# Performance work log

Measured on AMD Instinct MI355X. Metric: run time of the kernel, lower is better.

Reference implementation:

```python
import jax, jax.numpy as jnp
import numpy as np

MARGIN = 0.3
BIG = 9999999.0


def setup_inputs() -> dict:
    key = jax.random.key(0)
    k1, k2 = jax.random.split(key)
    emb = jax.random.normal(k1, (4096, 2048), dtype=jnp.float32)
    label = jax.random.randint(k2, (4096,), 0, 64, dtype=jnp.int64 if jax.config.jax_enable_x64 else jnp.int32)
    return {"emb": emb, "label": label}


def euclidean_dist(x, y):
    xx = jnp.sum(x * x, axis=1, keepdims=True)          # [m,1]
    yy = jnp.sum(y * y, axis=1, keepdims=True).T        # [1,n]
    dist = xx + yy - 2.0 * (x @ y.T)                    # [m,n]
    return jnp.sqrt(jnp.clip(dist, 1e-12, None))


def reference(emb, label):
    mat_dist = euclidean_dist(emb, emb)                 # [N,N]
    mat_sim = (label[:, None] == label[None, :]).astype(mat_dist.dtype)
    # batch-hard mining: top-1 of masked sorts == masked max / min reductions
    dist_ap = jnp.max(mat_dist - BIG * (1.0 - mat_sim), axis=1)  # hardest positive
    dist_an = jnp.min(mat_dist + BIG * mat_sim, axis=1)          # hardest negative
    # MarginRankingLoss(dist_an, dist_ap, y=1): mean(relu(margin - (dist_an - dist_ap)))
    loss = jnp.mean(jax.nn.relu(MARGIN - (dist_an - dist_ap)))
    prec = jnp.mean((dist_an > dist_ap).astype(jnp.float32))
    return (loss, prec)
```

## Files before the change

kernel.cpp:

```cpp
#include <hip/hip_runtime.h>

#define N_ROWS 4096
#define D_K    2048
#define BM 256
#define BK 64
#define NT (D_K / BK)
#define MARGIN 0.3f

typedef unsigned short u16;
typedef __attribute__((ext_vector_type(8))) short bf16x8;
typedef __attribute__((ext_vector_type(4))) float f32x4;

__device__ __forceinline__ void stage16(const u16* src, u16* dst) {
    __builtin_amdgcn_global_load_lds((const __attribute__((address_space(1))) unsigned int*)src,
                                     (__attribute__((address_space(3))) unsigned int*)dst, 16, 0, 0);
}

__device__ __forceinline__ u16 f2bf(float f) {
    unsigned u = __float_as_uint(f);
    u += 0x7fffu + ((u >> 16) & 1u);
    return (u16)(u >> 16);
}

__global__ __launch_bounds__(256) void prep_kernel(
    const float* __restrict__ emb, u16* __restrict__ embB,
    float* __restrict__ xx, unsigned* __restrict__ ap2, unsigned* __restrict__ an2)
{
    const int row = blockIdx.x;
    const int t = threadIdx.x;
    const float4* src = (const float4*)(emb + (size_t)row * D_K);
    ushort4* dst = (ushort4*)(embB + (size_t)row * D_K);
    float s = 0.f;
#pragma unroll
    for (int i = 0; i < 2; ++i) {
        float4 v = src[t + i * 256];
        s = fmaf(v.x, v.x, s);
        s = fmaf(v.y, v.y, s);
        s = fmaf(v.z, v.z, s);
        s = fmaf(v.w, v.w, s);
        ushort4 o;
        o.x = f2bf(v.x); o.y = f2bf(v.y); o.z = f2bf(v.z); o.w = f2bf(v.w);
        dst[t + i * 256] = o;
    }
#pragma unroll
    for (int off = 32; off >= 1; off >>= 1) s += __shfl_down(s, off, 64);
    __shared__ float red[4];
    if ((t & 63) == 0) red[t >> 6] = s;
    __syncthreads();
    if (t == 0) {
        xx[row] = red[0] + red[1] + red[2] + red[3];
        ap2[row] = 0u;
        an2[row] = 0x7f7fffffu;
    }
}

#define MM(mi, ni, ai, bi) \
    acc[mi][ni] = __builtin_amdgcn_mfma_f32_16x16x32_bf16(aq[ai][0], bq[bi][0], acc[mi][ni], 0, 0, 0); \
    acc[mi][ni] = __builtin_amdgcn_mfma_f32_16x16x32_bf16(aq[ai][1], bq[bi][1], acc[mi][ni], 0, 0, 0);

#define LDv(p) (*(const bf16x8*)(p))

#define STAGE_A(b, h, c, kt) stage16(gA + ((h) * 2 + (c)) * g64 + (kt), lA + ((b) * 16384 + ((h) * 128 + (c) * 64) * 64))
#define STAGE_B(b, q, kt)    stage16(gB + (q) * g64 + (kt),             lB + ((b) * 16384 + (q) * 4096))

#define BARRIER()  __builtin_amdgcn_s_barrier()
#define LGKM0()    asm volatile("s_waitcnt lgkmcnt(0)" ::: "memory")
#define VMW_(n)    asm volatile("s_waitcnt vmcnt(" #n ")" ::: "memory")
#define VMW(n)     VMW_(n)

#define KTILE(B_, NB_, KT1_, OKS_)                                                    \
  {                                                                                   \
    bf16x8 aq[4][2], bq[4][2];                                                        \
                    \
    aq[0][0] = LDv(AB + (B_)*32768 + aOff +    0 + kx0);                              \
    aq[0][1] = LDv(AB + (B_)*32768 + aOff +    0 + kx1);                              \
    aq[1][0] = LDv(AB + (B_)*32768 + aOff + 2048 + kx0);                              \
    aq[1][1] = LDv(AB + (B_)*32768 + aOff + 2048 + kx1);                              \
    aq[2][0] = LDv(AB + (B_)*32768 + aOff + 4096 + kx0);                              \
    aq[2][1] = LDv(AB + (B_)*32768 + aOff + 4096 + kx1);                              \
    aq[3][0] = LDv(AB + (B_)*32768 + aOff + 6144 + kx0);                              \
    aq[3][1] = LDv(AB + (B_)*32768 + aOff + 6144 + kx1);                              \
    bq[0][0] = LDv(BB + (B_)*32768 + bOff +    0 + kx0);                              \
    bq[0][1] = LDv(BB + (B_)*32768 + bOff +    0 + kx1);                              \
    bq[1][0] = LDv(BB + (B_)*32768 + bOff + 2048 + kx0);                              \
    bq[1][1] = LDv(BB + (B_)*32768 + bOff + 2048 + kx1);                              \
    if (OKS_) { STAGE_A(NB_, 0, 0, KT1_); STAGE_A(NB_, 1, 0, KT1_); }                 \
    asm volatile("s_waitcnt lgkmcnt(8)" ::: "memory");                                \
    BARRIER(); LGKM0();                                                               \
    __builtin_amdgcn_s_setprio(1);                                                    \
    MM(0, 0, 0, 0) MM(1, 1, 1, 1) MM(2, 0, 2, 0) MM(3, 1, 3, 1)                       \
    MM(0, 1, 0, 1) MM(1, 0, 1, 0) MM(2, 1, 2, 1) MM(3, 0, 3, 0)                       \
    __builtin_amdgcn_s_setprio(0);                                                    \
    if (OKS_) { VMW(4); } else { VMW(2); }                                            \
    BARRIER();                                                                        \
                 \
    bq[2][0] = LDv(BB + (B_)*32768 + bOff + 4096 + kx0);                              \
    bq[2][1] = LDv(BB + (B_)*32768 + bOff + 4096 + kx1);                              \
    bq[3][0] = LDv(BB + (B_)*32768 + bOff + 6144 + kx0);                              \
    bq[3][1] = LDv(BB + (B_)*32768 + bOff + 6144 + kx1);                              \
    if (OKS_) { STAGE_B(NB_, 0, KT1_); STAGE_B(NB_, 1, KT1_); }                       \
    BARRIER(); LGKM0();                                                               \
    __builtin_amdgcn_s_setprio(1);                                                    \
    MM(0, 2, 0, 2) MM(1, 3, 1, 3) MM(2, 2, 2, 2) MM(3, 3, 3, 3)                       \
    MM(0, 3, 0, 3) MM(1, 2, 1, 2) MM(2, 3, 2, 3) MM(3, 2, 3, 2)                       \
    __builtin_amdgcn_s_setprio(0);                                                    \
    if (OKS_) { VMW(4); } else { VMW(0); }                                            \
    BARRIER();                                                                        \
                      \
    aq[0][0] = LDv(AB + (B_)*32768 + aOff +  8192 + kx0);                             \
    aq[0][1] = LDv(AB + (B_)*32768 + aOff +  8192 + kx1);                             \
    aq[1][0] = LDv(AB + (B_)*32768 + aOff + 10240 + kx0);                             \
    aq[1][1] = LDv(AB + (B_)*32768 + aOff + 10240 + kx1);                             \
    aq[2][0] = LDv(AB + (B_)*32768 + aOff + 12288 + kx0);                             \
    aq[2][1] = LDv(AB + (B_)*32768 + aOff + 12288 + kx1);                             \
    aq[3][0] = LDv(AB + (B_)*32768 + aOff + 14336 + kx0);                             \
    aq[3][1] = LDv(AB + (B_)*32768 + aOff + 14336 + kx1);                             \
    if (OKS_) { STAGE_B(NB_, 2, KT1_); STAGE_B(NB_, 3, KT1_); }                       \
    BARRIER(); LGKM0();                                                               \
    __builtin_amdgcn_s_setprio(1);                                                    \
    MM(4, 2, 0, 2) MM(5, 3, 1, 3) MM(6, 2, 2, 2) MM(7, 3, 3, 3)                       \
    MM(4, 3, 0, 3) MM(5, 2, 1, 2) MM(6, 3, 2, 3) MM(7, 2, 3, 2)                       \
    __builtin_amdgcn_s_setprio(0);                                                    \
    BARRIER();                                                                        \
      \
    if (OKS_) { STAGE_A(NB_, 0, 1, KT1_); STAGE_A(NB_, 1, 1, KT1_); }                 \
    BARRIER();                                                                        \
    __builtin_amdgcn_s_setprio(1);                                                    \
    MM(4, 0, 0, 0) MM(5, 1, 1, 1) MM(6, 0, 2, 0) MM(7, 1, 3, 1)                       \
    MM(4, 1, 0, 1) MM(5, 0, 1, 0) MM(6, 1, 2, 1) MM(7, 0, 3, 0)                       \
    __builtin_amdgcn_s_setprio(0);                                                    \
    if (OKS_) { VMW(4); } else { VMW(0); }                                            \
    BARRIER();                                                                        \
  }

__global__ __launch_bounds__(512, 2) void gram_reduce_kernel(
    const u16* __restrict__ embB, const float* __restrict__ xx,
    const int* __restrict__ lab, unsigned* __restrict__ ap2, unsigned* __restrict__ an2)
{
    __shared__ u16 Ash[2 * BM * BK];
    __shared__ u16 Bsh[2 * BM * BK];
    __shared__ int labR[BM], labC[BM];
    __shared__ float xxR[BM], xxC[BM];

    const int tid = threadIdx.x;
    const int bid = blockIdx.x;
    const int swz = (bid & 7) * 32 + (bid >> 3);
    const int bm = swz >> 4, bn = swz & 15;
    const int row0 = bm * BM, col0 = bn * BM;

    const int csw = ((tid & 7) ^ ((tid >> 3) & 7)) * 8;
    const u16* gA = embB + (size_t)(row0 + (tid >> 3)) * D_K + csw;
    const u16* gB = embB + (size_t)(col0 + (tid >> 3)) * D_K + csw;
    u16* lA = Ash + tid * 8;
    u16* lB = Bsh + tid * 8;
    const size_t g64 = (size_t)64 * D_K;

    const int l = tid & 63, w = tid >> 6;
    const int wr = w >> 2, wc = w & 3;
    const int fr = l & 15, fkb = l >> 4;
    const int frs = fr & 7;
    const int kx0 = (fkb ^ frs) * 16;
    const int kx1 = kx0 ^ 64;
    const char* AB = (const char*)Ash;
    const char* BB = (const char*)Bsh;
    const int aOff = wr * 16384 + fr * 128;
    const int bOff = (wc >> 1) * 16384 + ((wc & 1) * 64 + fr) * 128;

    f32x4 acc[8][4];
#pragma unroll
    for (int m = 0; m < 8; ++m)
#pragma unroll
        for (int n = 0; n < 4; ++n) acc[m][n] = (f32x4){0.f, 0.f, 0.f, 0.f};

    STAGE_A(0, 0, 0, 0); STAGE_A(0, 1, 0, 0);
    STAGE_B(0, 0, 0); STAGE_B(0, 1, 0); STAGE_B(0, 2, 0); STAGE_B(0, 3, 0);
    STAGE_A(0, 0, 1, 0); STAGE_A(0, 1, 1, 0);
    VMW(4);
    BARRIER();

    for (int ii = 0; ii < NT / 2; ++ii) {
        const int kA = (2 * ii + 1) * BK;
        const int kB = (2 * ii + 2) * BK;
        const bool okB = (ii + 1 < NT / 2);
        KTILE(0, 1, kA, true)
        KTILE(1, 0, kB, okB)
    }

    if (tid < 256) { labR[tid] = lab[row0 + tid]; xxR[tid] = xx[row0 + tid]; }
    else           { int u2 = tid - 256; labC[u2] = lab[col0 + u2]; xxC[u2] = xx[col0 + u2]; }
    __syncthreads();

    const int rgrp = l >> 4;
#pragma unroll
    for (int m = 0; m < 8; ++m) {
#pragma unroll
        for (int r = 0; r < 4; ++r) {
            const int il = wr * 128 + m * 16 + rgrp * 4 + r;
            const int li = labR[il];
            const float xi = xxR[il];
            float apv = 0.f, anv = __FLT_MAX__;
#pragma unroll
            for (int n = 0; n < 4; ++n) {
                const int jl = wc * 64 + n * 16 + fr;
                float d2 = xi + xxC[jl] - 2.f * acc[m][n][r];
                d2 = fmaxf(d2, 1e-12f);
                const bool same = (labC[jl] == li);
                apv = same ? fmaxf(apv, d2) : apv;
                anv = same ? anv : fminf(anv, d2);
            }
#pragma unroll
            for (int off = 1; off < 16; off <<= 1) {
                apv = fmaxf(apv, __shfl_xor(apv, off, 64));
                anv = fminf(anv, __shfl_xor(anv, off, 64));
            }
            if (fr == 0) {
                atomicMax(&ap2[row0 + il], __float_as_uint(apv));
                atomicMin(&an2[row0 + il], __float_as_uint(anv));
            }
        }
    }
}

__global__ __launch_bounds__(256) void finalize_kernel(
    const unsigned* __restrict__ ap2, const unsigned* __restrict__ an2, float* __restrict__ out)
{
    const int t = threadIdx.x;
    float ls = 0.f, ps = 0.f;
    for (int i = t; i < N_ROWS; i += 256) {
        const float ap = sqrtf(__uint_as_float(ap2[i]));
        const float an = sqrtf(__uint_as_float(an2[i]));
        ls += fmaxf(MARGIN - an + ap, 0.f);
        ps += (an > ap) ? 1.f : 0.f;
    }
#pragma unroll
    for (int off = 32; off >= 1; off >>= 1) {
        ls += __shfl_down(ls, off, 64);
        ps += __shfl_down(ps, off, 64);
    }
    __shared__ float rl[4], rp[4];
    if ((t & 63) == 0) { rl[t >> 6] = ls; rp[t >> 6] = ps; }
    __syncthreads();
    if (t == 0) {
        out[0] = (rl[0] + rl[1] + rl[2] + rl[3]) * (1.f / N_ROWS);
        out[1] = (rp[0] + rp[1] + rp[2] + rp[3]) * (1.f / N_ROWS);
    }
}

extern "C" void kernel_launch(void* const* d_in, const int* in_sizes, int n_in,
                              void* d_out, int out_size, void* d_ws, size_t ws_size,
                              hipStream_t stream)
{
    const float* emb = (const float*)d_in[0];
    const int* lab = (const int*)d_in[1];
    float* out = (float*)d_out;

    char* ws = (char*)d_ws;
    u16* embB   = (u16*)ws;
    float* xx   = (float*)(ws + (size_t)N_ROWS * D_K * 2);
    unsigned* ap2 = (unsigned*)(ws + (size_t)N_ROWS * D_K * 2 + N_ROWS * 4);
    unsigned* an2 = (unsigned*)(ws + (size_t)N_ROWS * D_K * 2 + 2 * (size_t)N_ROWS * 4);

    prep_kernel<<<N_ROWS, 256, 0, stream>>>(emb, embB, xx, ap2, an2);
    dim3 grid((N_ROWS / BM) * (N_ROWS / BM));
    gram_reduce_kernel<<<grid, 512, 0, stream>>>(embB, xx, lab, ap2, an2);
    finalize_kernel<<<1, 256, 0, stream>>>(ap2, an2, out);
}
```

Measured before the change: 87.18 us.

## Switch GEMM main loop to BK=32 triple-buffered LDS pipeline

Replaces the two-stage BK=64 K-loop, which interleaved staging with four barrier-separated MFMA phases, with a simpler three-buffer ring of BK=32 tiles. Each step prefetches the tile two steps ahead, loads all A/B fragments once, and issues 32 MFMAs behind a single barrier. The aim is to hide global-to-LDS latency with deeper prefetch and cut the barrier count per unit of K. In exchange it runs twice as many K iterations, uses a narrower swizzle, and puts the prefetch and the next-tile reads under one vmcnt wait.

```diff
diff --git a/kernel.cpp b/kernel.cpp
--- a/kernel.cpp
+++ b/kernel.cpp
@@ -3,7 +3,7 @@
 #define N_ROWS 4096
 #define D_K    2048
 #define BM 256
-#define BK 64
+#define BK 32
 #define NT (D_K / BK)
 #define MARGIN 0.3f
 
@@ -54,82 +54,37 @@
     }
 }
 
-#define MM(mi, ni, ai, bi) \
-    acc[mi][ni] = __builtin_amdgcn_mfma_f32_16x16x32_bf16(aq[ai][0], bq[bi][0], acc[mi][ni], 0, 0, 0); \
-    acc[mi][ni] = __builtin_amdgcn_mfma_f32_16x16x32_bf16(aq[ai][1], bq[bi][1], acc[mi][ni], 0, 0, 0);
-
 #define LDv(p) (*(const bf16x8*)(p))
-
-#define STAGE_A(b, h, c, kt) stage16(gA + ((h) * 2 + (c)) * g64 + (kt), lA + ((b) * 16384 + ((h) * 128 + (c) * 64) * 64))
-#define STAGE_B(b, q, kt)    stage16(gB + (q) * g64 + (kt),             lB + ((b) * 16384 + (q) * 4096))
-
 #define BARRIER()  __builtin_amdgcn_s_barrier()
-#define LGKM0()    asm volatile("s_waitcnt lgkmcnt(0)" ::: "memory")
 #define VMW_(n)    asm volatile("s_waitcnt vmcnt(" #n ")" ::: "memory")
 #define VMW(n)     VMW_(n)
 
-#define KTILE(B_, NB_, KT1_, OKS_)                                                    \
+#define STAGE32(B3_, KTE_) do {                       \
+    stage16(gA0 + (KTE_), lA + (B3_) * 8192);         \
+    stage16(gA1 + (KTE_), lA + (B3_) * 8192 + 4096);  \
+    stage16(gB0 + (KTE_), lB + (B3_) * 8192);         \
+    stage16(gB1 + (KTE_), lB + (B3_) * 8192 + 4096);  \
+} while (0)
+
+#define KT32(B_, T_)                                                                  \
   {                                                                                   \
-    bf16x8 aq[4][2], bq[4][2];                                                        \
-                    \
-    aq[0][0] = LDv(AB + (B_)*32768 + aOff +    0 + kx0);                              \
-    aq[0][1] = LDv(AB + (B_)*32768 + aOff +    0 + kx1);                              \
-    aq[1][0] = LDv(AB + (B_)*32768 + aOff + 2048 + kx0);                              \
-    aq[1][1] = LDv(AB + (B_)*32768 + aOff + 2048 + kx1);                              \
-    aq[2][0] = LDv(AB + (B_)*32768 + aOff + 4096 + kx0);                              \
-    aq[2][1] = LDv(AB + (B_)*32768 + aOff + 4096 + kx1);                              \
-    aq[3][0] = LDv(AB + (B_)*32768 + aOff + 6144 + kx0);                              \
-    aq[3][1] = LDv(AB + (B_)*32768 + aOff + 6144 + kx1);                              \
-    bq[0][0] = LDv(BB + (B_)*32768 + bOff +    0 + kx0);                              \
-    bq[0][1] = LDv(BB + (B_)*32768 + bOff +    0 + kx1);                              \
-    bq[1][0] = LDv(BB + (B_)*32768 + bOff + 2048 + kx0);                              \
-    bq[1][1] = LDv(BB + (B_)*32768 + bOff + 2048 + kx1);                              \
-    if (OKS_) { STAGE_A(NB_, 0, 0, KT1_); STAGE_A(NB_, 1, 0, KT1_); }                 \
-    asm volatile("s_waitcnt lgkmcnt(8)" ::: "memory");                                \
-    BARRIER(); LGKM0();                                                               \
+    const bool ok = ((T_) + 2 < NT);                                                  \
+    if (ok) { STAGE32(((B_) + 2) % 3, ((T_) + 2) * BK); }                             \
+    bf16x8 aq[8], bq[4];                                                              \
+    _Pragma("unroll")                                                                 \
+    for (int n = 0; n < 4; ++n)                                                       \
+        bq[n] = LDv(BB + (B_) * 16384 + bOff + n * 1024 + kx);                        \
+    _Pragma("unroll")                                                                 \
+    for (int m = 0; m < 8; ++m)                                                       \
+        aq[m] = LDv(AB + (B_) * 16384 + aOff + m * 1024 + kx);                        \
     __builtin_amdgcn_s_setprio(1);                                                    \
-    MM(0, 0, 0, 0) MM(1, 1, 1, 1) MM(2, 0, 2, 0) MM(3, 1, 3, 1)                       \
-    MM(0, 1, 0, 1) MM(1, 0, 1, 0) MM(2, 1, 2, 1) MM(3, 0, 3, 0)                       \
+    _Pragma("unroll")                                                                 \
+    for (int m = 0; m < 8; ++m)                                                       \
+        _Pragma("unroll")                                                             \
+        for (int n = 0; n < 4; ++n)                                                   \
+            acc[m][n] = __builtin_amdgcn_mfma_f32_16x16x32_bf16(aq[m], bq[n], acc[m][n], 0, 0, 0); \
     __builtin_amdgcn_s_setprio(0);                                                    \
-    if (OKS_) { VMW(4); } else { VMW(2); }                                            \
-    BARRIER();                                                                        \
-                 \
-    bq[2][0] = LDv(BB + (B_)*32768 + bOff + 4096 + kx0);                              \
-    bq[2][1] = LDv(BB + (B_)*32768 + bOff + 4096 + kx1);                              \
-    bq[3][0] = LDv(BB + (B_)*32768 + bOff + 6144 + kx0);                              \
-    bq[3][1] = LDv(BB + (B_)*32768 + bOff + 6144 + kx1);                              \
-    if (OKS_) { STAGE_B(NB_, 0, KT1_); STAGE_B(NB_, 1, KT1_); }                       \
-    BARRIER(); LGKM0();                                                               \
-    __builtin_amdgcn_s_setprio(1);                                                    \
-    MM(0, 2, 0, 2) MM(1, 3, 1, 3) MM(2, 2, 2, 2) MM(3, 3, 3, 3)                       \
-    MM(0, 3, 0, 3) MM(1, 2, 1, 2) MM(2, 3, 2, 3) MM(3, 2, 3, 2)                       \
-    __builtin_amdgcn_s_setprio(0);                                                    \
-    if (OKS_) { VMW(4); } else { VMW(0); }                                            \
-    BARRIER();                                                                        \
-                      \
-    aq[0][0] = LDv(AB + (B_)*32768 + aOff +  8192 + kx0);                             \
-    aq[0][1] = LDv(AB + (B_)*32768 + aOff +  8192 + kx1);                             \
-    aq[1][0] = LDv(AB + (B_)*32768 + aOff + 10240 + kx0);                             \
-    aq[1][1] = LDv(AB + (B_)*32768 + aOff + 10240 + kx1);                             \
-    aq[2][0] = LDv(AB + (B_)*32768 + aOff + 12288 + kx0);                             \
-    aq[2][1] = LDv(AB + (B_)*32768 + aOff + 12288 + kx1);                             \
-    aq[3][0] = LDv(AB + (B_)*32768 + aOff + 14336 + kx0);                             \
-    aq[3][1] = LDv(AB + (B_)*32768 + aOff + 14336 + kx1);                             \
-    if (OKS_) { STAGE_B(NB_, 2, KT1_); STAGE_B(NB_, 3, KT1_); }                       \
-    BARRIER(); LGKM0();                                                               \
-    __builtin_amdgcn_s_setprio(1);                                                    \
-    MM(4, 2, 0, 2) MM(5, 3, 1, 3) MM(6, 2, 2, 2) MM(7, 3, 3, 3)                       \
-    MM(4, 3, 0, 3) MM(5, 2, 1, 2) MM(6, 3, 2, 3) MM(7, 2, 3, 2)                       \
-    __builtin_amdgcn_s_setprio(0);                                                    \
-    BARRIER();                                                                        \
-      \
-    if (OKS_) { STAGE_A(NB_, 0, 1, KT1_); STAGE_A(NB_, 1, 1, KT1_); }                 \
-    BARRIER();                                                                        \
-    __builtin_amdgcn_s_setprio(1);                                                    \
-    MM(4, 0, 0, 0) MM(5, 1, 1, 1) MM(6, 0, 2, 0) MM(7, 1, 3, 1)                       \
-    MM(4, 1, 0, 1) MM(5, 0, 1, 0) MM(6, 1, 2, 1) MM(7, 0, 3, 0)                       \
-    __builtin_amdgcn_s_setprio(0);                                                    \
-    if (OKS_) { VMW(4); } else { VMW(0); }                                            \
+    if (ok) { VMW(4); } else { VMW(0); }                                              \
     BARRIER();                                                                        \
   }
 
@@ -137,8 +92,8 @@
     const u16* __restrict__ embB, const float* __restrict__ xx,
     const int* __restrict__ lab, unsigned* __restrict__ ap2, unsigned* __restrict__ an2)
 {
-    __shared__ u16 Ash[2 * BM * BK];
-    __shared__ u16 Bsh[2 * BM * BK];
+    __shared__ u16 Ash[3 * BM * BK];
+    __shared__ u16 Bsh[3 * BM * BK];
     __shared__ int labR[BM], labC[BM];
     __shared__ float xxR[BM], xxC[BM];
 
@@ -148,23 +103,23 @@
     const int bm = swz >> 4, bn = swz & 15;
     const int row0 = bm * BM, col0 = bn * BM;
 
-    const int csw = ((tid & 7) ^ ((tid >> 3) & 7)) * 8;
-    const u16* gA = embB + (size_t)(row0 + (tid >> 3)) * D_K + csw;
-    const u16* gB = embB + (size_t)(col0 + (tid >> 3)) * D_K + csw;
+    const int csw = ((tid & 3) ^ ((tid >> 2) & 3)) * 8;
+    const int srow = tid >> 2;
+    const u16* gA0 = embB + (size_t)(row0 + srow) * D_K + csw;
+    const u16* gA1 = embB + (size_t)(row0 + 128 + srow) * D_K + csw;
+    const u16* gB0 = embB + (size_t)(col0 + srow) * D_K + csw;
+    const u16* gB1 = embB + (size_t)(col0 + 128 + srow) * D_K + csw;
     u16* lA = Ash + tid * 8;
     u16* lB = Bsh + tid * 8;
-    const size_t g64 = (size_t)64 * D_K;
 
     const int l = tid & 63, w = tid >> 6;
     const int wr = w >> 2, wc = w & 3;
     const int fr = l & 15, fkb = l >> 4;
-    const int frs = fr & 7;
-    const int kx0 = (fkb ^ frs) * 16;
-    const int kx1 = kx0 ^ 64;
+    const int kx = ((fkb ^ (fr & 3)) * 16);
     const char* AB = (const char*)Ash;
     const char* BB = (const char*)Bsh;
-    const int aOff = wr * 16384 + fr * 128;
-    const int bOff = (wc >> 1) * 16384 + ((wc & 1) * 64 + fr) * 128;
+    const int aOff = wr * 8192 + fr * 64;
+    const int bOff = (wc >> 1) * 8192 + (wc & 1) * 4096 + fr * 64;
 
     f32x4 acc[8][4];
 #pragma unroll
@@ -172,19 +127,18 @@
 #pragma unroll
         for (int n = 0; n < 4; ++n) acc[m][n] = (f32x4){0.f, 0.f, 0.f, 0.f};
 
-    STAGE_A(0, 0, 0, 0); STAGE_A(0, 1, 0, 0);
-    STAGE_B(0, 0, 0); STAGE_B(0, 1, 0); STAGE_B(0, 2, 0); STAGE_B(0, 3, 0);
-    STAGE_A(0, 0, 1, 0); STAGE_A(0, 1, 1, 0);
+    STAGE32(0, 0);
+    STAGE32(1, BK);
     VMW(4);
     BARRIER();
 
-    for (int ii = 0; ii < NT / 2; ++ii) {
-        const int kA = (2 * ii + 1) * BK;
-        const int kB = (2 * ii + 2) * BK;
-        const bool okB = (ii + 1 < NT / 2);
-        KTILE(0, 1, kA, true)
-        KTILE(1, 0, kB, okB)
-    }
+    for (int ii = 0; ii < 21; ++ii) {
+        const int t3 = 3 * ii;
+        KT32(0, t3)
+        KT32(1, t3 + 1)
+        KT32(2, t3 + 2)
+    }
+    KT32(0, 63)
 
     if (tid < 256) { labR[tid] = lab[row0 + tid]; xxR[tid] = xx[row0 + tid]; }
     else           { int u2 = tid - 256; labC[u2] = lab[col0 + u2]; xxC[u2] = xx[col0 + u2]; }
```

After: 91.49 us. 1.05x slower.
